# Kernel optimization log

Measured on AMD Instinct MI355X. Metric: run time of the kernel, lower is better.

The kernel has to match this reference:

```python
import jax, jax.numpy as jnp
import numpy as np


def setup_inputs() -> dict:
    key = jax.random.key(0)
    k_v, k_w = jax.random.split(key)
    L, N, H, D = 2048, 8, 16, 64
    v = jax.random.normal(k_v, (N, L, H, D), dtype=jnp.float32)
    # torch init: self.w.data.uniform_(-0.1, 0.1) overwrites the sorted randn
    w = jax.random.uniform(k_w, (L,), dtype=jnp.float32, minval=-0.1, maxval=0.1)
    return {"v": v, "w": w}


def _toeplitz_bias(w):
    # Faithful to _construnct_bias: p = [flip(w[1:]), w], bias[i, j] = p[L-1 - i + j]
    # which is the symmetric Toeplitz matrix bias[i, j] = w[|i - j|].
    L = w.shape[0]
    idx = jnp.abs(jnp.arange(L)[:, None] - jnp.arange(L)[None, :])  # [L, L]
    return w[idx]


def reference(v, w):
    # PositionalBias._naive
    L = w.shape[0]
    bias = _toeplitz_bias(w)                      # [L, L]
    z_pb = bias.sum(-1).reshape(1, L, 1)          # [1, L, 1]
    pbv = jnp.einsum('nlhd,lj->njhd', v, bias)    # [N, L, H, D]
    return pbv, z_pb
```

## Files before the change

kernel.cpp:

```cpp
#include <hip/hip_runtime.h>
#include <hip/hip_bf16.h>

#define L 2048
#define HD 1024
#define NB 8
#define NT 32
#define PROW 4096

using f32x4 = __attribute__((ext_vector_type(4))) float;
using fl4   = __attribute__((ext_vector_type(4))) float;
using s16x8 = __attribute__((ext_vector_type(8))) short;

__device__ __forceinline__ short f2bf(float f) {
    __hip_bfloat16 h = __float2bfloat16(f);
    short s;
    __builtin_memcpy(&s, &h, 2);
    return s;
}

__device__ __forceinline__ void gload_lds16(const void* g, void* l) {
    __builtin_amdgcn_global_load_lds(
        (const __attribute__((address_space(1))) unsigned int*)g,
        (__attribute__((address_space(3))) unsigned int*)l, 16, 0, 0);
}

__global__ __launch_bounds__(256) void pb_prep(const float* __restrict__ w,
                                               short* __restrict__ p8) {
    int idx = blockIdx.x * 256 + threadIdx.x;
    int s = idx >> 12;
    int x = idx & (PROW - 1);
    int k = x + s;
    short val = 0;
    if (k <= 4094) {
        int d = k - 2047; d = d < 0 ? -d : d;
        val = f2bf(w[d]);
    }
    p8[idx] = val;
}

__global__ __launch_bounds__(256) void pb_vtile(const float* __restrict__ v,
                                                s16x8* __restrict__ vtile) {
    __shared__ __align__(16) short Ts[256 * 64];
    const int kk = blockIdx.x, cm = blockIdx.y, n = blockIdx.z;
    const int l0 = kk * 64, c0 = cm * 256;
    const int t = threadIdx.x;
    const float* vn = v + (size_t)n * L * HD;

    #pragma unroll
    for (int i = 0; i < 16; ++i) {
        int unit = i * 256 + t;
        int l = unit >> 6, cq = unit & 63;
        fl4 x = *(const fl4*)&vn[(size_t)(l0 + l) * HD + c0 + cq * 4];
        int lsub = l & 7, lblk = l >> 3;
        #pragma unroll
        for (int j = 0; j < 4; ++j) {
            int c = cq * 4 + j;
            Ts[c * 64 + ((lblk ^ ((c >> 2) & 7)) << 3) + lsub] = f2bf(x[j]);
        }
    }
    __syncthreads();

    s16x8* outtile = vtile + ((size_t)((n * 4 + cm) * NT + kk)) * 2048;
    #pragma unroll
    for (int i2 = 0; i2 < 8; ++i2) {
        int ci = i2 * 256 + t;
        int nh = ci >> 10, cih = ci & 1023;
        int seg = cih >> 8, o = cih & 255;
        int c = seg * 64 + nh * 32 + (o >> 3), s = o & 7;
        int h = s ^ (c & 7);
        int slot = h ^ ((c >> 2) & 7);
        outtile[ci] = *(const s16x8*)&Ts[c * 64 + slot * 8];
    }
}

__global__ __launch_bounds__(512, 2) void pb_gemm8(const short* __restrict__ p8,
                                                   const short* __restrict__ vtile,
                                                   float* __restrict__ out) {
    __shared__ __align__(16) short lds_[65536];

    const int bid = blockIdx.x;
    const int cmn = bid & 31;
    const int jm  = bid >> 5;
    const int cm  = cmn & 3;
    const int n   = cmn >> 2;
    const int j0 = jm * 256;
    const int c0 = cm * 256;

    const int t = threadIdx.x;
    const int lane = t & 63;
    const int w = t >> 6;
    const int wr = w >> 2, wc = w & 3;
    const int fr = lane & 15, fk = lane >> 4;

    int offA[8], offB[4];
    #pragma unroll
    for (int m = 0; m < 8; ++m) {
        int r = wr * 128 + m * 16 + fr;
        offA[m] = r * 128 + ((fk ^ (r & 7)) << 4);
    }
    #pragma unroll
    for (int nf = 0; nf < 4; ++nf) {
        int c = wc * 64 + nf * 16 + fr;
        offB[nf] = c * 128 + ((fk ^ (c & 7)) << 4);
    }

    auto mkA = [&](int mh, int rho) {
        int dc = rho * 1024 + mh * 512 + w * 64 + lane;
        int r = dc >> 3, s = dc & 7, h = s ^ (r & 7);
        int q = 2047 + h * 8 - j0 - r;
        int srow = q & 7;
        return p8 + srow * PROW + (q - srow);
    };
    const short* srcA0_0 = mkA(0, 0); const short* srcA0_1 = mkA(0, 1);
    const short* srcA1_0 = mkA(1, 0); const short* srcA1_1 = mkA(1, 1);

    const short* vb = vtile + ((size_t)((n * 4 + cm) * NT)) * 2048 * 8;
    const short* srcB0_0 = vb + ((w) * 64 + lane) * 8;
    const short* srcB0_1 = vb + ((w + 8) * 64 + lane) * 8;
    const short* srcB1_0 = vb + (1024 + (w) * 64 + lane) * 8;
    const short* srcB1_1 = vb + (1024 + (w + 8) * 64 + lane) * 8;

    const int dA0 = w * 1024, dA1 = 16384 + w * 1024;
    const int dB0 = 32768 + (w >> 2) * 8192 + (w & 3) * 1024;
    const int dB1 = dB0 + 16384;

#define STAGE_ALL(base) { \
    gload_lds16(srcA0_0, (char*)lds_ + (base) + dA0); \
    gload_lds16(srcA0_1, (char*)lds_ + (base) + dA1); \
    gload_lds16(srcA1_0, (char*)lds_ + (base) + 8192 + dA0); \
    gload_lds16(srcA1_1, (char*)lds_ + (base) + 8192 + dA1); \
    gload_lds16(srcB0_0, (char*)lds_ + (base) + dB0); \
    gload_lds16(srcB0_1, (char*)lds_ + (base) + dB1); \
    gload_lds16(srcB1_0, (char*)lds_ + (base) + 4096 + dB0); \
    gload_lds16(srcB1_1, (char*)lds_ + (base) + 4096 + dB1); \
    srcA0_0 += 64; srcA0_1 += 64; srcA1_0 += 64; srcA1_1 += 64; \
    srcB0_0 += 16384; srcB0_1 += 16384; srcB1_0 += 16384; srcB1_1 += 16384; }

    STAGE_ALL(0);
    __syncthreads();

    f32x4 acc[8][4] = {};

    for (int T = 0; T < NT; ++T) {
        const char* bR = (const char*)lds_ + (T & 1) * 65536;

        if (T < NT - 1) {
            const int nb = ((T + 1) & 1) * 65536;
            STAGE_ALL(nb);
        }

        s16x8 af[4][2], bf0[2][2], bf1[2][2];

        #pragma unroll
        for (int m = 0; m < 4; ++m) {
            af[m][0] = *(const s16x8*)(bR + offA[m]);
            af[m][1] = *(const s16x8*)(bR + (offA[m] ^ 64));
        }
        #pragma unroll
        for (int nf = 0; nf < 2; ++nf) {
            bf0[nf][0] = *(const s16x8*)(bR + 32768 + offB[nf]);
            bf0[nf][1] = *(const s16x8*)(bR + 32768 + (offB[nf] ^ 64));
        }
        #pragma unroll
        for (int m = 0; m < 4; ++m)
            #pragma unroll
            for (int nf = 0; nf < 2; ++nf)
                #pragma unroll
                for (int ki = 0; ki < 2; ++ki)
                    acc[m][nf] = __builtin_amdgcn_mfma_f32_16x16x32_bf16(
                        af[m][ki], bf0[nf][ki], acc[m][nf], 0, 0, 0);

        #pragma unroll
        for (int nf = 0; nf < 2; ++nf) {
            bf1[nf][0] = *(const s16x8*)(bR + 32768 + offB[2 + nf]);
            bf1[nf][1] = *(const s16x8*)(bR + 32768 + (offB[2 + nf] ^ 64));
        }
        #pragma unroll
        for (int m = 0; m < 4; ++m)
            #pragma unroll
            for (int nf = 0; nf < 2; ++nf)
                #pragma unroll
                for (int ki = 0; ki < 2; ++ki)
                    acc[m][2 + nf] = __builtin_amdgcn_mfma_f32_16x16x32_bf16(
                        af[m][ki], bf1[nf][ki], acc[m][2 + nf], 0, 0, 0);

        #pragma unroll
        for (int m = 0; m < 4; ++m) {
            af[m][0] = *(const s16x8*)(bR + offA[4 + m]);
            af[m][1] = *(const s16x8*)(bR + (offA[4 + m] ^ 64));
        }
        #pragma unroll
        for (int m = 0; m < 4; ++m)
            #pragma unroll
            for (int nf = 0; nf < 2; ++nf)
                #pragma unroll
                for (int ki = 0; ki < 2; ++ki)
                    acc[4 + m][nf] = __builtin_amdgcn_mfma_f32_16x16x32_bf16(
                        af[m][ki], bf0[nf][ki], acc[4 + m][nf], 0, 0, 0);

        #pragma unroll
        for (int m = 0; m < 4; ++m)
            #pragma unroll
            for (int nf = 0; nf < 2; ++nf)
                #pragma unroll
                for (int ki = 0; ki < 2; ++ki)
                    acc[4 + m][2 + nf] = __builtin_amdgcn_mfma_f32_16x16x32_bf16(
                        af[m][ki], bf1[nf][ki], acc[4 + m][2 + nf], 0, 0, 0);

        __syncthreads();
    }

    float* outn = out + (size_t)n * L * HD;
    #pragma unroll
    for (int m = 0; m < 8; ++m) {
        const int row = j0 + wr * 128 + m * 16 + fk * 4;
        #pragma unroll
        for (int nf = 0; nf < 4; ++nf) {
            const int col = c0 + wc * 64 + nf * 16 + fr;
            #pragma unroll
            for (int r = 0; r < 4; ++r)
                outn[(size_t)(row + r) * HD + col] = acc[m][nf][r];
        }
    }
}

__global__ __launch_bounds__(256) void pb_z(const float* __restrict__ w,
                                            float* __restrict__ z) {
    __shared__ float part[256];
    __shared__ float S[L];
    const int t = threadIdx.x;
    float loc[8]; float s = 0.f;
    #pragma unroll
    for (int i = 0; i < 8; ++i) { loc[i] = w[t * 8 + i]; s += loc[i]; }
    part[t] = s;
    __syncthreads();
    if (t == 0) {
        float a = 0.f;
        for (int i = 0; i < 256; ++i) { float tmp = part[i]; part[i] = a; a += tmp; }
    }
    __syncthreads();
    float a = part[t];
    #pragma unroll
    for (int i = 0; i < 8; ++i) { a += loc[i]; S[t * 8 + i] = a; }
    __syncthreads();
    const float w0 = S[0];
    #pragma unroll
    for (int i = 0; i < 8; ++i) {
        int j = t * 8 + i;
        z[j] = S[j] + S[2047 - j] - w0;
    }
}

extern "C" void kernel_launch(void* const* d_in, const int* in_sizes, int n_in,
                              void* d_out, int out_size, void* d_ws, size_t ws_size,
                              hipStream_t stream) {
    const float* v = (const float*)d_in[0];
    const float* w = (const float*)d_in[1];
    float* out = (float*)d_out;

    short* p8    = (short*)d_ws;
    short* vtile = (short*)((char*)d_ws + 65536);

    pb_prep<<<128, 256, 0, stream>>>(w, p8);
    pb_vtile<<<dim3(NT, 4, NB), 256, 0, stream>>>(v, (s16x8*)vtile);
    pb_gemm8<<<256, 512, 0, stream>>>(p8, vtile, out);
    pb_z<<<1, 256, 0, stream>>>(w, out + (size_t)NB * L * HD);
}
```

Before: 81.58 us.

## Shrink GEMM tiles to 128x128 with 4-wave blocks and new V layout

Replaces the 256x256-tile, 512-thread GEMM with a 128x128-tile, 256-thread kernel launched as 1024 blocks, halving LDS per block. The V tile layout is reorganized so each block stages its 128-column slice with per-lane swizzled addresses. It also raises wave priority around the MFMA block with s_setprio. The aim is more blocks and better occupancy and load balance across CUs, traded against lower arithmetic intensity and more global/LDS traffic per FLOP.

```diff
diff --git a/kernel.cpp b/kernel.cpp
--- a/kernel.cpp
+++ b/kernel.cpp
@@ -39,10 +39,10 @@
 }
 
 __global__ __launch_bounds__(256) void pb_vtile(const float* __restrict__ v,
-                                                s16x8* __restrict__ vtile) {
+                                                s16x8* __restrict__ vt) {
     __shared__ __align__(16) short Ts[256 * 64];
-    const int kk = blockIdx.x, cm = blockIdx.y, n = blockIdx.z;
-    const int l0 = kk * 64, c0 = cm * 256;
+    const int kk = blockIdx.x, cg4 = blockIdx.y, n = blockIdx.z;
+    const int l0 = kk * 64, c0 = cg4 * 256;
     const int t = threadIdx.x;
     const float* vn = v + (size_t)n * L * HD;
 
@@ -60,160 +60,133 @@
     }
     __syncthreads();
 
-    s16x8* outtile = vtile + ((size_t)((n * 4 + cm) * NT + kk)) * 2048;
+    s16x8* outp = vt + ((size_t)(n * NT + kk) * 1024 + c0) * 8;
     #pragma unroll
     for (int i2 = 0; i2 < 8; ++i2) {
         int ci = i2 * 256 + t;
-        int nh = ci >> 10, cih = ci & 1023;
-        int seg = cih >> 8, o = cih & 255;
-        int c = seg * 64 + nh * 32 + (o >> 3), s = o & 7;
-        int h = s ^ (c & 7);
+        int c = ci >> 3, h = ci & 7;
         int slot = h ^ ((c >> 2) & 7);
-        outtile[ci] = *(const s16x8*)&Ts[c * 64 + slot * 8];
-    }
-}
-
-__global__ __launch_bounds__(512, 2) void pb_gemm8(const short* __restrict__ p8,
-                                                   const short* __restrict__ vtile,
+        outp[ci] = *(const s16x8*)&Ts[c * 64 + slot * 8];
+    }
+}
+
+__global__ __launch_bounds__(256, 2) void pb_gemm4(const short* __restrict__ p8,
+                                                   const short* __restrict__ vt,
                                                    float* __restrict__ out) {
-    __shared__ __align__(16) short lds_[65536];
+    __shared__ __align__(16) short lds_[32768];
 
     const int bid = blockIdx.x;
-    const int cmn = bid & 31;
-    const int jm  = bid >> 5;
-    const int cm  = cmn & 3;
-    const int n   = cmn >> 2;
-    const int j0 = jm * 256;
-    const int c0 = cm * 256;
+    const int cm = bid & 7;
+    const int n  = (bid >> 3) & 7;
+    const int jm = bid >> 6;
+    const int j0 = jm * 128;
+    const int c0 = cm * 128;
 
     const int t = threadIdx.x;
     const int lane = t & 63;
     const int w = t >> 6;
-    const int wr = w >> 2, wc = w & 3;
+    const int wr = w >> 1, wc = w & 1;
     const int fr = lane & 15, fk = lane >> 4;
 
-    int offA[8], offB[4];
-    #pragma unroll
-    for (int m = 0; m < 8; ++m) {
-        int r = wr * 128 + m * 16 + fr;
+    int offA[4], offB[4];
+    #pragma unroll
+    for (int m = 0; m < 4; ++m) {
+        int r = wr * 64 + m * 16 + fr;
         offA[m] = r * 128 + ((fk ^ (r & 7)) << 4);
     }
     #pragma unroll
     for (int nf = 0; nf < 4; ++nf) {
         int c = wc * 64 + nf * 16 + fr;
-        offB[nf] = c * 128 + ((fk ^ (c & 7)) << 4);
-    }
-
-    auto mkA = [&](int mh, int rho) {
-        int dc = rho * 1024 + mh * 512 + w * 64 + lane;
-        int r = dc >> 3, s = dc & 7, h = s ^ (r & 7);
-        int q = 2047 + h * 8 - j0 - r;
-        int srow = q & 7;
-        return p8 + srow * PROW + (q - srow);
-    };
-    const short* srcA0_0 = mkA(0, 0); const short* srcA0_1 = mkA(0, 1);
-    const short* srcA1_0 = mkA(1, 0); const short* srcA1_1 = mkA(1, 1);
-
-    const short* vb = vtile + ((size_t)((n * 4 + cm) * NT)) * 2048 * 8;
-    const short* srcB0_0 = vb + ((w) * 64 + lane) * 8;
-    const short* srcB0_1 = vb + ((w + 8) * 64 + lane) * 8;
-    const short* srcB1_0 = vb + (1024 + (w) * 64 + lane) * 8;
-    const short* srcB1_1 = vb + (1024 + (w + 8) * 64 + lane) * 8;
-
-    const int dA0 = w * 1024, dA1 = 16384 + w * 1024;
-    const int dB0 = 32768 + (w >> 2) * 8192 + (w & 3) * 1024;
-    const int dB1 = dB0 + 16384;
+        offB[nf] = 16384 + c * 128 + ((fk ^ (c & 7)) << 4);
+    }
+
+    const short* srcA0; const short* srcA1; const short* srcA2; const short* srcA3;
+    const short* srcB0; const short* srcB1; const short* srcB2; const short* srcB3;
+    {
+        const size_t bbase = ((size_t)(n * NT) * 1024 + c0) * 8ull;
+        int dc, r, s, h, q, srow, c;
+        dc = w * 256 + 0 * 64 + lane;
+        r = dc >> 3; s = dc & 7; h = s ^ (r & 7);
+        q = 2047 + h * 8 - j0 - r; srow = q & 7;
+        srcA0 = p8 + srow * PROW + (q - srow);
+        c = dc >> 3; h = (dc & 7) ^ (c & 7);
+        srcB0 = (const short*)(vt + (bbase + (size_t)c * 8 + h) * 8);
+        dc = w * 256 + 1 * 64 + lane;
+        r = dc >> 3; s = dc & 7; h = s ^ (r & 7);
+        q = 2047 + h * 8 - j0 - r; srow = q & 7;
+        srcA1 = p8 + srow * PROW + (q - srow);
+        c = dc >> 3; h = (dc & 7) ^ (c & 7);
+        srcB1 = (const short*)(vt + (bbase + (size_t)c * 8 + h) * 8);
+        dc = w * 256 + 2 * 64 + lane;
+        r = dc >> 3; s = dc & 7; h = s ^ (r & 7);
+        q = 2047 + h * 8 - j0 - r; srow = q & 7;
+        srcA2 = p8 + srow * PROW + (q - srow);
+        c = dc >> 3; h = (dc & 7) ^ (c & 7);
+        srcB2 = (const short*)(vt + (bbase + (size_t)c * 8 + h) * 8);
+        dc = w * 256 + 3 * 64 + lane;
+        r = dc >> 3; s = dc & 7; h = s ^ (r & 7);
+        q = 2047 + h * 8 - j0 - r; srow = q & 7;
+        srcA3 = p8 + srow * PROW + (q - srow);
+        c = dc >> 3; h = (dc & 7) ^ (c & 7);
+        srcB3 = (const short*)(vt + (bbase + (size_t)c * 8 + h) * 8);
+    }
+    const int wA = w * 4096;
 
 #define STAGE_ALL(base) { \
-    gload_lds16(srcA0_0, (char*)lds_ + (base) + dA0); \
-    gload_lds16(srcA0_1, (char*)lds_ + (base) + dA1); \
-    gload_lds16(srcA1_0, (char*)lds_ + (base) + 8192 + dA0); \
-    gload_lds16(srcA1_1, (char*)lds_ + (base) + 8192 + dA1); \
-    gload_lds16(srcB0_0, (char*)lds_ + (base) + dB0); \
-    gload_lds16(srcB0_1, (char*)lds_ + (base) + dB1); \
-    gload_lds16(srcB1_0, (char*)lds_ + (base) + 4096 + dB0); \
-    gload_lds16(srcB1_1, (char*)lds_ + (base) + 4096 + dB1); \
-    srcA0_0 += 64; srcA0_1 += 64; srcA1_0 += 64; srcA1_1 += 64; \
-    srcB0_0 += 16384; srcB0_1 += 16384; srcB1_0 += 16384; srcB1_1 += 16384; }
+    gload_lds16(srcA0, (char*)lds_ + (base) + wA); \
+    gload_lds16(srcA1, (char*)lds_ + (base) + wA + 1024); \
+    gload_lds16(srcA2, (char*)lds_ + (base) + wA + 2048); \
+    gload_lds16(srcA3, (char*)lds_ + (base) + wA + 3072); \
+    gload_lds16(srcB0, (char*)lds_ + (base) + 16384 + wA); \
+    gload_lds16(srcB1, (char*)lds_ + (base) + 16384 + wA + 1024); \
+    gload_lds16(srcB2, (char*)lds_ + (base) + 16384 + wA + 2048); \
+    gload_lds16(srcB3, (char*)lds_ + (base) + 16384 + wA + 3072); \
+    srcA0 += 64; srcA1 += 64; srcA2 += 64; srcA3 += 64; \
+    srcB0 += 65536; srcB1 += 65536; srcB2 += 65536; srcB3 += 65536; }
 
     STAGE_ALL(0);
     __syncthreads();
 
-    f32x4 acc[8][4] = {};
+    f32x4 acc[4][4] = {};
 
     for (int T = 0; T < NT; ++T) {
-        const char* bR = (const char*)lds_ + (T & 1) * 65536;
+        const char* bR = (const char*)lds_ + (T & 1) * 32768;
 
         if (T < NT - 1) {
-            const int nb = ((T + 1) & 1) * 65536;
+            const int nb = ((T + 1) & 1) * 32768;
             STAGE_ALL(nb);
         }
 
-        s16x8 af[4][2], bf0[2][2], bf1[2][2];
-
+        s16x8 af[4][2], bf[4][2];
         #pragma unroll
         for (int m = 0; m < 4; ++m) {
             af[m][0] = *(const s16x8*)(bR + offA[m]);
             af[m][1] = *(const s16x8*)(bR + (offA[m] ^ 64));
         }
         #pragma unroll
-        for (int nf = 0; nf < 2; ++nf) {
-            bf0[nf][0] = *(const s16x8*)(bR + 32768 + offB[nf]);
-            bf0[nf][1] = *(const s16x8*)(bR + 32768 + (offB[nf] ^ 64));
-        }
+        for (int nf = 0; nf < 4; ++nf) {
+            bf[nf][0] = *(const s16x8*)(bR + offB[nf]);
+            bf[nf][1] = *(const s16x8*)(bR + (offB[nf] ^ 64));
+        }
+
+        __builtin_amdgcn_s_setprio(1);
         #pragma unroll
         for (int m = 0; m < 4; ++m)
             #pragma unroll
-            for (int nf = 0; nf < 2; ++nf)
+            for (int nf = 0; nf < 4; ++nf)
                 #pragma unroll
                 for (int ki = 0; ki < 2; ++ki)
                     acc[m][nf] = __builtin_amdgcn_mfma_f32_16x16x32_bf16(
-                        af[m][ki], bf0[nf][ki], acc[m][nf], 0, 0, 0);
-
-        #pragma unroll
-        for (int nf = 0; nf < 2; ++nf) {
-            bf1[nf][0] = *(const s16x8*)(bR + 32768 + offB[2 + nf]);
-            bf1[nf][1] = *(const s16x8*)(bR + 32768 + (offB[2 + nf] ^ 64));
-        }
-        #pragma unroll
-        for (int m = 0; m < 4; ++m)
-            #pragma unroll
-            for (int nf = 0; nf < 2; ++nf)
-                #pragma unroll
-                for (int ki = 0; ki < 2; ++ki)
-                    acc[m][2 + nf] = __builtin_amdgcn_mfma_f32_16x16x32_bf16(
-                        af[m][ki], bf1[nf][ki], acc[m][2 + nf], 0, 0, 0);
-
-        #pragma unroll
-        for (int m = 0; m < 4; ++m) {
-            af[m][0] = *(const s16x8*)(bR + offA[4 + m]);
-            af[m][1] = *(const s16x8*)(bR + (offA[4 + m] ^ 64));
-        }
-        #pragma unroll
-        for (int m = 0; m < 4; ++m)
-            #pragma unroll
-            for (int nf = 0; nf < 2; ++nf)
-                #pragma unroll
-                for (int ki = 0; ki < 2; ++ki)
-                    acc[4 + m][nf] = __builtin_amdgcn_mfma_f32_16x16x32_bf16(
-                        af[m][ki], bf0[nf][ki], acc[4 + m][nf], 0, 0, 0);
-
-        #pragma unroll
-        for (int m = 0; m < 4; ++m)
-            #pragma unroll
-            for (int nf = 0; nf < 2; ++nf)
-                #pragma unroll
-                for (int ki = 0; ki < 2; ++ki)
-                    acc[4 + m][2 + nf] = __builtin_amdgcn_mfma_f32_16x16x32_bf16(
-                        af[m][ki], bf1[nf][ki], acc[4 + m][2 + nf], 0, 0, 0);
+                        af[m][ki], bf[nf][ki], acc[m][nf], 0, 0, 0);
+        __builtin_amdgcn_s_setprio(0);
 
         __syncthreads();
     }
 
     float* outn = out + (size_t)n * L * HD;
     #pragma unroll
-    for (int m = 0; m < 8; ++m) {
-        const int row = j0 + wr * 128 + m * 16 + fk * 4;
+    for (int m = 0; m < 4; ++m) {
+        const int row = j0 + wr * 64 + m * 16 + fk * 4;
         #pragma unroll
         for (int nf = 0; nf < 4; ++nf) {
             const int col = c0 + wc * 64 + nf * 16 + fr;
@@ -258,11 +231,11 @@
     const float* w = (const float*)d_in[1];
     float* out = (float*)d_out;
 
-    short* p8    = (short*)d_ws;
-    short* vtile = (short*)((char*)d_ws + 65536);
+    short* p8 = (short*)d_ws;
+    s16x8* vt = (s16x8*)((char*)d_ws + 65536);
 
     pb_prep<<<128, 256, 0, stream>>>(w, p8);
-    pb_vtile<<<dim3(NT, 4, NB), 256, 0, stream>>>(v, (s16x8*)vtile);
-    pb_gemm8<<<256, 512, 0, stream>>>(p8, vtile, out);
+    pb_vtile<<<dim3(NT, 4, NB), 256, 0, stream>>>(v, vt);
+    pb_gemm4<<<1024, 256, 0, stream>>>(p8, (const short*)vt, out);
     pb_z<<<1, 256, 0, stream>>>(w, out + (size_t)NB * L * HD);
 }
```

Measured after the change: 84.51 us. 3.6% more time.
